# Kernel tuning notes

Hardware: AMD Instinct MI355X
Metric: run time of the kernel (lower is better)

## Reference

```python
import jax, jax.numpy as jnp
import numpy as np

N_NODES = 100000
N_EDGES = 1600000
IN_DIM = 128
HID = 128
EMB = 64


def _glorot(key, shape):
    fan_in, fan_out = shape[0], shape[1]
    lim = np.sqrt(6.0 / (fan_in + fan_out))
    return jax.random.uniform(key, shape, jnp.float32, -lim, lim)


def setup_inputs() -> dict:
    key = jax.random.key(0)
    ks = jax.random.split(key, 16)
    x = jax.random.normal(ks[0], (N_NODES, IN_DIM), jnp.float32)
    src = jax.random.randint(ks[1], (N_EDGES,), 0, N_NODES, jnp.int64)
    dst = jax.random.randint(ks[2], (N_EDGES,), 0, N_NODES, jnp.int64)
    # GCN encoder weights (GraphConv: weight [in,out], bias [out])
    W1 = _glorot(ks[3], (IN_DIM, HID)); b1 = jnp.zeros((HID,), jnp.float32)
    W2 = _glorot(ks[4], (HID, EMB)); b2 = jnp.zeros((EMB,), jnp.float32)
    # MLP predictor: 2*EMB=128 -> 64 -> 32 -> 1
    Wp1 = _glorot(ks[5], (2 * EMB, 64)); bp1 = jnp.zeros((64,), jnp.float32)
    Wp2 = _glorot(ks[6], (64, 32)); bp2 = jnp.zeros((32,), jnp.float32)
    Wp3 = _glorot(ks[7], (32, 1)); bp3 = jnp.zeros((1,), jnp.float32)
    return {"x": x, "src": src, "dst": dst,
            "W1": W1, "b1": b1, "W2": W2, "b2": b2,
            "Wp1": Wp1, "bp1": bp1, "Wp2": Wp2, "bp2": bp2,
            "Wp3": Wp3, "bp3": bp3}


def _gcn_conv(x, src, dst, W, b, n_nodes):
    # DGL GraphConv, norm='both': symmetric degree normalization, sum aggregation.
    ones = jnp.ones((src.shape[0],), x.dtype)
    deg_out = jnp.clip(jax.ops.segment_sum(ones, src, num_segments=n_nodes), 1.0)
    deg_in = jnp.clip(jax.ops.segment_sum(ones, dst, num_segments=n_nodes), 1.0)
    h = (x * jax.lax.rsqrt(deg_out)[:, None]) @ W          # [N, out]
    agg = jax.ops.segment_sum(h[src], dst, num_segments=n_nodes)  # gather + scatter-add
    return agg * jax.lax.rsqrt(deg_in)[:, None] + b


def reference(x, src, dst, W1, b1, W2, b2, Wp1, bp1, Wp2, bp2, Wp3, bp3):
    n = x.shape[0]
    h = jax.nn.relu(_gcn_conv(x, src, dst, W1, b1, n))   # layer 1 (with activation)
    h = _gcn_conv(h, src, dst, W2, b2, n)                # layer 2 (no activation)
    # edge-wise concat of endpoint embeddings: [E, 2*EMB]
    emb = jnp.concatenate([h[src], h[dst]], axis=1)
    z = jax.nn.relu(emb @ Wp1 + bp1)
    z = jax.nn.relu(z @ Wp2 + bp2)
    score = z @ Wp3 + bp3                                # [E, 1]
    return jax.nn.sigmoid(score)
```

## Files before the change

### kernel.cpp

```cpp
#include <hip/hip_runtime.h>
#include <math.h>


#define NBLK 256
#define NBUK 512
#define GRD (NBUK * NBLK)
#define GRT (2 * GRD)

typedef __attribute__((ext_vector_type(8))) short bf16x8;
typedef __attribute__((ext_vector_type(4))) float f32x4;

__device__ __forceinline__ float bl(unsigned u) { return __uint_as_float(u << 16); }
__device__ __forceinline__ float bh(unsigned u) { return __uint_as_float(u & 0xffff0000u); }
__device__ __forceinline__ unsigned short f2bf(float f) {
  unsigned u = __float_as_uint(f);
  return (unsigned short)((u + 0x7fffu + ((u >> 16) & 1u)) >> 16);
}
__device__ __forceinline__ unsigned packbf2(float a, float b) {
  return (unsigned)f2bf(a) | ((unsigned)f2bf(b) << 16);
}


__global__ __launch_bounds__(256) void k_hist(
    const int* __restrict__ src, const int* __restrict__ dst,
    int* __restrict__ grams, int E,
    const float* __restrict__ W1, const float* __restrict__ W2,
    const float* __restrict__ Wp1, const float* __restrict__ Wp2,
    unsigned short* __restrict__ W1t, unsigned short* __restrict__ W2t,
    unsigned short* __restrict__ Wct, unsigned short* __restrict__ Wp2t) {
  __shared__ int hd[NBUK], hs[NBUK];
  int blk = blockIdx.x, t = threadIdx.x;
  {
    int i = blk * 256 + t;
    if (i < 16384) {
      int n = i >> 7, k = i & 127;
      W1t[i] = f2bf(W1[k * 128 + n]);
    } else if (i < 24576) {
      int j = i - 16384; int n = j >> 7, k = j & 127;
      W2t[j] = f2bf(W2[k * 64 + n]);
    } else if (i < 32768) {
      int j = i - 24576; int c = j >> 6, k = j & 63;
      float v = (c < 64) ? Wp1[k * 64 + c] : Wp1[(k + 64) * 64 + (c - 64)];
      Wct[j] = f2bf(v);
    } else if (i < 34816) {
      int j = i - 32768; int n = j >> 6, k = j & 63;
      Wp2t[j] = f2bf(Wp2[k * 32 + n]);
    }
  }
  for (int k = t; k < NBUK; k += 256) { hd[k] = 0; hs[k] = 0; }
  __syncthreads();
  int chunk = (E + NBLK - 1) / NBLK;
  int start = blk * chunk, end = min(E, start + chunk);
  for (int i = start + t; i < end; i += 256) {
    atomicAdd(&hd[dst[i] >> 8], 1);
    atomicAdd(&hs[src[i] >> 8], 1);
  }
  __syncthreads();
  for (int k = t; k < NBUK; k += 256) {
    grams[k * NBLK + blk] = hd[k];
    grams[GRD + k * NBLK + blk] = hs[k];
  }
}

__global__ __launch_bounds__(256) void k_gscan1(const int* __restrict__ g,
                                                int* __restrict__ bsum) {
  __shared__ int lds[256];
  int b = blockIdx.x, t = threadIdx.x;
  int base = b * 1024 + t * 4;
  int s = g[base] + g[base + 1] + g[base + 2] + g[base + 3];
  lds[t] = s; __syncthreads();
  for (int st = 128; st > 0; st >>= 1) {
    if (t < st) lds[t] += lds[t + st];
    __syncthreads();
  }
  if (t == 0) bsum[b] = lds[0];
}

__global__ __launch_bounds__(256) void k_gscan3(int* __restrict__ g,
                                                const int* __restrict__ bsum) {
  __shared__ int lds[256], lds2[256];
  int b = blockIdx.x, t = threadIdx.x;
  int bv = bsum[t];
  lds2[t] = bv; __syncthreads();
  for (int st = 1; st < 256; st <<= 1) {
    int add = (t >= st) ? lds2[t - st] : 0;
    __syncthreads();
    lds2[t] += add;
    __syncthreads();
  }
  int bpref = (b > 0) ? lds2[b - 1] : 0;

  int base = b * 1024 + t * 4;
  int v[4]; int s = 0;
#pragma unroll
  for (int j = 0; j < 4; j++) { v[j] = g[base + j]; s += v[j]; }
  lds[t] = s; __syncthreads();
  int mine = s;
  for (int st = 1; st < 256; st <<= 1) {
    int add = (t >= st) ? lds[t - st] : 0;
    __syncthreads();
    lds[t] += add;
    __syncthreads();
  }
  int excl = lds[t] - mine + bpref;
#pragma unroll
  for (int j = 0; j < 4; j++) { g[base + j] = excl; excl += v[j]; }
}

__global__ __launch_bounds__(256) void k_part(
    const int* __restrict__ src, const int* __restrict__ dst,
    const int* __restrict__ grams, unsigned* __restrict__ pdst,
    unsigned char* __restrict__ sbuf, int E) {
  __shared__ int curd[NBUK], curs[NBUK];
  int blk = blockIdx.x, t = threadIdx.x;
  for (int k = t; k < NBUK; k += 256) {
    curd[k] = grams[k * NBLK + blk];
    curs[k] = grams[GRD + k * NBLK + blk] - E;
  }
  __syncthreads();
  int chunk = (E + NBLK - 1) / NBLK;
  int start = blk * chunk, end = min(E, start + chunk);
  for (int i = start + t; i < end; i += 256) {
    int s = src[i], d = dst[i];
    int pd = atomicAdd(&curd[d >> 8], 1);
    pdst[pd] = ((unsigned)s << 8) | (unsigned)(d & 255);
    int ps = atomicAdd(&curs[s >> 8], 1);
    sbuf[ps] = (unsigned char)(s & 255);
  }
}

__global__ __launch_bounds__(256) void k_dcsr(
    const unsigned* __restrict__ pdst, const unsigned char* __restrict__ sbuf,
    const int* __restrict__ grams,
    int* __restrict__ adj, int* __restrict__ rowst,
    float* __restrict__ rin, float* __restrict__ rout, int N, int E) {
  __shared__ int hist[256], cur[256];
  int b = blockIdx.x, t = threadIdx.x;
  int base = grams[b * 256];
  int end  = grams[b * 256 + 256];
  hist[t] = 0; __syncthreads();
  for (int i = base + t; i < end; i += 256)
    atomicAdd(&hist[pdst[i] & 255], 1);
  __syncthreads();
  int cnt = hist[t];
  for (int st = 1; st < 256; st <<= 1) {
    int add = (t >= st) ? hist[t - st] : 0;
    __syncthreads();
    hist[t] += add;
    __syncthreads();
  }
  int excl = hist[t] - cnt;
  cur[t] = excl;
  int node = b * 256 + t;
  if (node < N) {
    rowst[node] = base + excl;
    rin[node] = rsqrtf((float)max(cnt, 1));
  }
  __syncthreads();
  for (int i = base + t; i < end; i += 256) {
    unsigned u = pdst[i];
    int pos = base + atomicAdd(&cur[u & 255], 1);
    adj[pos] = (int)(u >> 8);
  }
  __syncthreads();
  hist[t] = 0; __syncthreads();
  int sb = grams[GRD + b * 256] - E;
  int se = grams[GRD + b * 256 + 256] - E;
  for (int i = sb + t; i < se; i += 256)
    atomicAdd(&hist[sbuf[i]], 1);
  __syncthreads();
  if (node < N) rout[node] = rsqrtf((float)max(hist[t], 1));
}

template <int K, int BN, bool ABF, bool SC>
__global__ __launch_bounds__(256) void k_gemm(
    const void* __restrict__ Av, const float* __restrict__ scale,
    const unsigned short* __restrict__ Wt, unsigned short* __restrict__ C, int M) {
  constexpr int KP = K + 8;
  __shared__ __attribute__((aligned(16))) unsigned short As[64][KP];
  __shared__ __attribute__((aligned(16))) unsigned short Ws[BN][KP];
  int tid = threadIdx.x;
  int row0 = blockIdx.x * 64;

  for (int i = tid; i < BN * K / 8; i += 256) {
    int n = i / (K / 8), seg = i % (K / 8);
    *(uint4*)&Ws[n][seg * 8] = ((const uint4*)Wt)[i];
  }
  {
    constexpr int CH = K / 4;
    int r = tid >> 2, q = tid & 3;
    int row = row0 + r;
    if (row < M) {
      float sc = SC ? scale[row] : 1.0f;
      if constexpr (!ABF) {
        const float4* ap = (const float4*)((const float*)Av + (size_t)row * K + q * CH);
#pragma unroll
        for (int c = 0; c < CH / 8; c++) {
          float4 v0 = ap[2 * c], v1 = ap[2 * c + 1];
          uint4 o;
          o.x = packbf2(v0.x * sc, v0.y * sc);
          o.y = packbf2(v0.z * sc, v0.w * sc);
          o.z = packbf2(v1.x * sc, v1.y * sc);
          o.w = packbf2(v1.z * sc, v1.w * sc);
          *(uint4*)&As[r][q * CH + c * 8] = o;
        }
      } else {
        const uint4* ap = (const uint4*)((const unsigned short*)Av + (size_t)row * K + q * CH);
#pragma unroll
        for (int c = 0; c < CH / 8; c++) {
          uint4 v = ap[c];
          if constexpr (SC) {
            uint4 o;
            o.x = packbf2(bl(v.x) * sc, bh(v.x) * sc);
            o.y = packbf2(bl(v.y) * sc, bh(v.y) * sc);
            o.z = packbf2(bl(v.z) * sc, bh(v.z) * sc);
            o.w = packbf2(bl(v.w) * sc, bh(v.w) * sc);
            *(uint4*)&As[r][q * CH + c * 8] = o;
          } else {
            *(uint4*)&As[r][q * CH + c * 8] = v;
          }
        }
      }
    } else {
#pragma unroll
      for (int c = 0; c < CH / 8; c++)
        *(uint4*)&As[r][q * CH + c * 8] = make_uint4(0, 0, 0, 0);
    }
  }
  __syncthreads();

  constexpr int KS = K / 32;
  constexpr int NT = BN / 16;
  int wav = tid >> 6, lane = tid & 63;
  int quad = lane >> 4, lrow = lane & 15;
  int mb = wav * 16;

  bf16x8 af[KS];
#pragma unroll
  for (int s = 0; s < KS; s++)
    af[s] = *(const bf16x8*)&As[mb + lrow][s * 32 + quad * 8];

  f32x4 acc[NT];
#pragma unroll
  for (int nt = 0; nt < NT; nt++) acc[nt] = (f32x4){0.f, 0.f, 0.f, 0.f};
#pragma unroll
  for (int nt = 0; nt < NT; nt++) {
#pragma unroll
    for (int s = 0; s < KS; s++) {
      bf16x8 bf = *(const bf16x8*)&Ws[nt * 16 + lrow][s * 32 + quad * 8];
      acc[nt] = __builtin_amdgcn_mfma_f32_16x16x32_bf16(af[s], bf, acc[nt], 0, 0, 0);
    }
  }
#pragma unroll
  for (int nt = 0; nt < NT; nt++) {
#pragma unroll
    for (int reg = 0; reg < 4; reg++) {
      int row = row0 + mb + quad * 4 + reg;
      if (row < M) C[(size_t)row * BN + nt * 16 + lrow] = f2bf(acc[nt][reg]);
    }
  }
}

template <int F>
__global__ __launch_bounds__(256) void k_agg(
    const unsigned short* __restrict__ hin, const int* __restrict__ rowst,
    const int* __restrict__ adj, const float* __restrict__ rin,
    const float* __restrict__ bias, unsigned short* __restrict__ hout,
    int N, int E, int do_relu) {
  constexpr int TPN = F / 8;
  constexpr int NPB = 256 / TPN;
  int node = blockIdx.x * NPB + threadIdx.x / TPN;
  int c = threadIdx.x % TPN;
  if (node >= N) return;
  int start = rowst[node];
  int end = (node + 1 < N) ? rowst[node + 1] : E;
  const uint4* h4 = (const uint4*)hin;

  float a[8], b[8];
#pragma unroll
  for (int j = 0; j < 8; j++) { a[j] = 0.f; b[j] = 0.f; }

  int i = start;
  for (; i + 3 < end; i += 4) {
    uint4 w0 = h4[(size_t)adj[i] * TPN + c];
    uint4 w1 = h4[(size_t)adj[i + 1] * TPN + c];
    uint4 w2 = h4[(size_t)adj[i + 2] * TPN + c];
    uint4 w3 = h4[(size_t)adj[i + 3] * TPN + c];
    a[0] += bl(w0.x); a[1] += bh(w0.x); a[2] += bl(w0.y); a[3] += bh(w0.y);
    a[4] += bl(w0.z); a[5] += bh(w0.z); a[6] += bl(w0.w); a[7] += bh(w0.w);
    b[0] += bl(w1.x); b[1] += bh(w1.x); b[2] += bl(w1.y); b[3] += bh(w1.y);
    b[4] += bl(w1.z); b[5] += bh(w1.z); b[6] += bl(w1.w); b[7] += bh(w1.w);
    a[0] += bl(w2.x); a[1] += bh(w2.x); a[2] += bl(w2.y); a[3] += bh(w2.y);
    a[4] += bl(w2.z); a[5] += bh(w2.z); a[6] += bl(w2.w); a[7] += bh(w2.w);
    b[0] += bl(w3.x); b[1] += bh(w3.x); b[2] += bl(w3.y); b[3] += bh(w3.y);
    b[4] += bl(w3.z); b[5] += bh(w3.z); b[6] += bl(w3.w); b[7] += bh(w3.w);
  }
  for (; i < end; i++) {
    uint4 w0 = h4[(size_t)adj[i] * TPN + c];
    a[0] += bl(w0.x); a[1] += bh(w0.x); a[2] += bl(w0.y); a[3] += bh(w0.y);
    a[4] += bl(w0.z); a[5] += bh(w0.z); a[6] += bl(w0.w); a[7] += bh(w0.w);
  }
  float r = rin[node];
  const float4* bp = (const float4*)(bias + c * 8);
  float4 bb0 = bp[0], bb1 = bp[1];
  float o0 = fmaf(a[0] + b[0], r, bb0.x);
  float o1 = fmaf(a[1] + b[1], r, bb0.y);
  float o2 = fmaf(a[2] + b[2], r, bb0.z);
  float o3 = fmaf(a[3] + b[3], r, bb0.w);
  float o4 = fmaf(a[4] + b[4], r, bb1.x);
  float o5 = fmaf(a[5] + b[5], r, bb1.y);
  float o6 = fmaf(a[6] + b[6], r, bb1.z);
  float o7 = fmaf(a[7] + b[7], r, bb1.w);
  if (do_relu) {
    o0 = fmaxf(o0, 0.f); o1 = fmaxf(o1, 0.f); o2 = fmaxf(o2, 0.f);
    o3 = fmaxf(o3, 0.f); o4 = fmaxf(o4, 0.f); o5 = fmaxf(o5, 0.f);
    o6 = fmaxf(o6, 0.f); o7 = fmaxf(o7, 0.f);
  }
  uint4 o;
  o.x = packbf2(o0, o1); o.y = packbf2(o2, o3);
  o.z = packbf2(o4, o5); o.w = packbf2(o6, o7);
  ((uint4*)hout)[(size_t)node * TPN + c] = o;
}

__global__ __launch_bounds__(256) void k_edge(
    const unsigned short* __restrict__ ab, const int* __restrict__ src,
    const int* __restrict__ dst,
    const unsigned short* __restrict__ Wp2t, const float* __restrict__ bp1,
    const float* __restrict__ bp2, const float* __restrict__ Wp3,
    const float* __restrict__ bp3, float* __restrict__ out, int E) {
  __shared__ __attribute__((aligned(16))) unsigned short z1s[128][72];
  __shared__ __attribute__((aligned(16))) unsigned short w2t[32][72];
  __shared__ float sb1[64], sb2[32], sw3[32];

  int t = threadIdx.x;
  {
    uint4 v = ((const uint4*)Wp2t)[t];
    int n = t >> 3, seg = t & 7;
    *(uint4*)&w2t[n][seg * 8] = v;
    if (t < 64) sb1[t] = bp1[t];
    else if (t < 96) sb2[t - 64] = bp2[t - 64];
    else if (t < 128) sw3[t - 96] = Wp3[t - 96];
  }
  __syncthreads();

  int p0 = blockIdx.x * 128;
  {
    int m = t >> 1, half = t & 1, p = p0 + m;
    int s = 0, d = 0;
    if (p < E) { s = src[p]; d = dst[p]; }
    const uint4* apf = (const uint4*)(ab + (size_t)s * 128 + half * 32);
    const uint4* bpf = (const uint4*)(ab + (size_t)d * 128 + 64 + half * 32);
    int jb = half * 32;
#pragma unroll
    for (int q = 0; q < 4; q++) {
      uint4 av = apf[q], bv = bpf[q];
      int j = jb + 8 * q;
      float z0 = fmaxf(bl(av.x) + bl(bv.x) + sb1[j + 0], 0.f);
      float z1 = fmaxf(bh(av.x) + bh(bv.x) + sb1[j + 1], 0.f);
      float z2 = fmaxf(bl(av.y) + bl(bv.y) + sb1[j + 2], 0.f);
      float z3 = fmaxf(bh(av.y) + bh(bv.y) + sb1[j + 3], 0.f);
      float z4 = fmaxf(bl(av.z) + bl(bv.z) + sb1[j + 4], 0.f);
      float z5 = fmaxf(bh(av.z) + bh(bv.z) + sb1[j + 5], 0.f);
      float z6 = fmaxf(bl(av.w) + bl(bv.w) + sb1[j + 6], 0.f);
      float z7 = fmaxf(bh(av.w) + bh(bv.w) + sb1[j + 7], 0.f);
      uint4 o;
      o.x = packbf2(z0, z1); o.y = packbf2(z2, z3);
      o.z = packbf2(z4, z5); o.w = packbf2(z6, z7);
      *(uint4*)&z1s[m][j] = o;
    }
  }
  __syncthreads();

  int wav = t >> 6, lane = t & 63;
  int quad = lane >> 4, lrow = lane & 15;

  bf16x8 bfr[2][2];
#pragma unroll
  for (int s = 0; s < 2; s++)
#pragma unroll
    for (int nt = 0; nt < 2; nt++)
      bfr[s][nt] = *(const bf16x8*)&w2t[nt * 16 + lrow][s * 32 + quad * 8];

  f32x4 acc[2][2];
#pragma unroll
  for (int mt = 0; mt < 2; mt++)
#pragma unroll
    for (int nt = 0; nt < 2; nt++) acc[mt][nt] = (f32x4){0.f, 0.f, 0.f, 0.f};

#pragma unroll
  for (int mt = 0; mt < 2; mt++) {
    int mb = (wav * 2 + mt) * 16;
#pragma unroll
    for (int s = 0; s < 2; s++) {
      bf16x8 a = *(const bf16x8*)&z1s[mb + lrow][s * 32 + quad * 8];
#pragma unroll
      for (int nt = 0; nt < 2; nt++)
        acc[mt][nt] = __builtin_amdgcn_mfma_f32_16x16x32_bf16(a, bfr[s][nt], acc[mt][nt], 0, 0, 0);
    }
  }

  float bb0 = sb2[lrow], bb1 = sb2[16 + lrow];
  float w30 = sw3[lrow], w31 = sw3[16 + lrow];
  float p2[2][4];
#pragma unroll
  for (int mt = 0; mt < 2; mt++)
#pragma unroll
    for (int reg = 0; reg < 4; reg++)
      p2[mt][reg] = fmaxf(acc[mt][0][reg] + bb0, 0.f) * w30 +
                    fmaxf(acc[mt][1][reg] + bb1, 0.f) * w31;
#pragma unroll
  for (int off = 1; off < 16; off <<= 1) {
#pragma unroll
    for (int mt = 0; mt < 2; mt++)
#pragma unroll
      for (int reg = 0; reg < 4; reg++)
        p2[mt][reg] += __shfl_xor(p2[mt][reg], off, 64);
  }
  if (lrow < 4) {
    float b3 = bp3[0];
#pragma unroll
    for (int mt = 0; mt < 2; mt++) {
      float score = p2[mt][0];
      if (lrow == 1) score = p2[mt][1];
      if (lrow == 2) score = p2[mt][2];
      if (lrow == 3) score = p2[mt][3];
      score += b3;
      int pp = p0 + (wav * 2 + mt) * 16 + quad * 4 + lrow;
      if (pp < E) out[pp] = 1.0f / (1.0f + __expf(-score));
    }
  }
}

extern "C" void kernel_launch(void* const* d_in, const int* in_sizes, int n_in,
                              void* d_out, int out_size, void* d_ws, size_t ws_size,
                              hipStream_t stream) {
  const float* x   = (const float*)d_in[0];
  const int*   src = (const int*)d_in[1];
  const int*   dst = (const int*)d_in[2];
  const float* W1  = (const float*)d_in[3];
  const float* b1  = (const float*)d_in[4];
  const float* W2  = (const float*)d_in[5];
  const float* b2  = (const float*)d_in[6];
  const float* Wp1 = (const float*)d_in[7];
  const float* bp1 = (const float*)d_in[8];
  const float* Wp2 = (const float*)d_in[9];
  const float* bp2 = (const float*)d_in[10];
  const float* Wp3 = (const float*)d_in[11];
  const float* bp3 = (const float*)d_in[12];
  float* out = (float*)d_out;

  int N = in_sizes[0] / 128;
  int E = in_sizes[1];

  char* w = (char*)d_ws;
  unsigned short* bufA = (unsigned short*)w;
  unsigned* pdst = (unsigned*)w;
  unsigned char* sbuf = (unsigned char*)(w + (size_t)E * 4);
  w += (size_t)N * 128 * 2;
  unsigned short* bufB = (unsigned short*)w; w += (size_t)N * 128 * 2;
  int* grams  = (int*)w;    w += (size_t)GRT * sizeof(int);
  int* bsum   = (int*)w;    w += 256 * sizeof(int);
  int* rowst  = (int*)w;    w += (size_t)N * sizeof(int);
  int* adj    = (int*)w;    w += (size_t)E * sizeof(int);
  float* rin  = (float*)w;  w += (size_t)N * sizeof(float);
  float* rout = (float*)w;  w += (size_t)N * sizeof(float);
  unsigned short* W1t  = (unsigned short*)w; w += 16384 * 2;
  unsigned short* W2t  = (unsigned short*)w; w += 8192 * 2;
  unsigned short* Wct  = (unsigned short*)w; w += 8192 * 2;
  unsigned short* Wp2t = (unsigned short*)w; w += 2048 * 2;

  int nbk = (N + 255) / 256;

  k_hist<<<NBLK, 256, 0, stream>>>(src, dst, grams, E, W1, W2, Wp1, Wp2,
                                   W1t, W2t, Wct, Wp2t);
  k_gscan1<<<GRT / 1024, 256, 0, stream>>>(grams, bsum);
  k_gscan3<<<GRT / 1024, 256, 0, stream>>>(grams, bsum);
  k_part<<<NBLK, 256, 0, stream>>>(src, dst, grams, pdst, sbuf, E);
  k_dcsr<<<nbk, 256, 0, stream>>>(pdst, sbuf, grams, adj, rowst, rin, rout, N, E);

  k_gemm<128, 128, false, true><<<(N + 63) / 64, 256, 0, stream>>>(x, rout, W1t, bufA, N);
  k_agg<128><<<(N + 15) / 16, 256, 0, stream>>>(bufA, rowst, adj, rin, b1, bufB, N, E, 1);
  k_gemm<128, 64, true, true><<<(N + 63) / 64, 256, 0, stream>>>(bufB, rout, W2t, bufA, N);
  k_agg<64><<<(N + 31) / 32, 256, 0, stream>>>(bufA, rowst, adj, rin, b2, bufB, N, E, 0);
  k_gemm<64, 128, true, false><<<(N + 63) / 64, 256, 0, stream>>>(bufB, nullptr, Wct, bufA, N);
  k_edge<<<(E + 127) / 128, 256, 0, stream>>>(bufA, src, dst, Wp2t,
                                              bp1, bp2, Wp3, bp3, out, E);
}
```

Before: 378.5 us.

## Process edge MLP in destination-sorted CSR order and scatter scores back

Result: slower. 395.7 us (+4.6%).

```diff
diff --git a/kernel.cpp b/kernel.cpp
--- a/kernel.cpp
+++ b/kernel.cpp
@@ -109,7 +109,7 @@
 
 __global__ __launch_bounds__(256) void k_part(
     const int* __restrict__ src, const int* __restrict__ dst,
-    const int* __restrict__ grams, unsigned* __restrict__ pdst,
+    const int* __restrict__ grams, uint2* __restrict__ pdst,
     unsigned char* __restrict__ sbuf, int E) {
   __shared__ int curd[NBUK], curs[NBUK];
   int blk = blockIdx.x, t = threadIdx.x;
@@ -123,24 +123,25 @@
   for (int i = start + t; i < end; i += 256) {
     int s = src[i], d = dst[i];
     int pd = atomicAdd(&curd[d >> 8], 1);
-    pdst[pd] = ((unsigned)s << 8) | (unsigned)(d & 255);
+    pdst[pd] = make_uint2((unsigned)s, (unsigned)i | ((unsigned)(d & 255) << 21));
     int ps = atomicAdd(&curs[s >> 8], 1);
     sbuf[ps] = (unsigned char)(s & 255);
   }
 }
 
 __global__ __launch_bounds__(256) void k_dcsr(
-    const unsigned* __restrict__ pdst, const unsigned char* __restrict__ sbuf,
+    const uint2* __restrict__ pdst, const unsigned char* __restrict__ sbuf,
     const int* __restrict__ grams,
-    int* __restrict__ adj, int* __restrict__ rowst,
-    float* __restrict__ rin, float* __restrict__ rout, int N, int E) {
+    int* __restrict__ adj, int* __restrict__ dnode, int* __restrict__ eidx,
+    int* __restrict__ rowst, float* __restrict__ rin, float* __restrict__ rout,
+    int N, int E) {
   __shared__ int hist[256], cur[256];
   int b = blockIdx.x, t = threadIdx.x;
   int base = grams[b * 256];
   int end  = grams[b * 256 + 256];
   hist[t] = 0; __syncthreads();
   for (int i = base + t; i < end; i += 256)
-    atomicAdd(&hist[pdst[i] & 255], 1);
+    atomicAdd(&hist[(pdst[i].y >> 21) & 255], 1);
   __syncthreads();
   int cnt = hist[t];
   for (int st = 1; st < 256; st <<= 1) {
@@ -158,9 +159,13 @@
   }
   __syncthreads();
   for (int i = base + t; i < end; i += 256) {
-    unsigned u = pdst[i];
-    int pos = base + atomicAdd(&cur[u & 255], 1);
-    adj[pos] = (int)(u >> 8);
+    uint2 u = pdst[i];
+    int lo = (u.y >> 21) & 255;
+    int eid = (int)(u.y & 0x1FFFFFu);
+    int pos = base + atomicAdd(&cur[lo], 1);
+    adj[pos] = (int)u.x;
+    dnode[pos] = b * 256 + lo;
+    eidx[pos] = eid;
   }
   __syncthreads();
   hist[t] = 0; __syncthreads();
@@ -323,11 +328,11 @@
 }
 
 __global__ __launch_bounds__(256) void k_edge(
-    const unsigned short* __restrict__ ab, const int* __restrict__ src,
-    const int* __restrict__ dst,
+    const unsigned short* __restrict__ ab, const int* __restrict__ adj,
+    const int* __restrict__ dnode,
     const unsigned short* __restrict__ Wp2t, const float* __restrict__ bp1,
     const float* __restrict__ bp2, const float* __restrict__ Wp3,
-    const float* __restrict__ bp3, float* __restrict__ out, int E) {
+    const float* __restrict__ bp3, float* __restrict__ tmp, int E) {
   __shared__ __attribute__((aligned(16))) unsigned short z1s[128][72];
   __shared__ __attribute__((aligned(16))) unsigned short w2t[32][72];
   __shared__ float sb1[64], sb2[32], sw3[32];
@@ -347,7 +352,7 @@
   {
     int m = t >> 1, half = t & 1, p = p0 + m;
     int s = 0, d = 0;
-    if (p < E) { s = src[p]; d = dst[p]; }
+    if (p < E) { s = adj[p]; d = dnode[p]; }
     const uint4* apf = (const uint4*)(ab + (size_t)s * 128 + half * 32);
     const uint4* bpf = (const uint4*)(ab + (size_t)d * 128 + 64 + half * 32);
     int jb = half * 32;
@@ -426,9 +431,16 @@
       if (lrow == 3) score = p2[mt][3];
       score += b3;
       int pp = p0 + (wav * 2 + mt) * 16 + quad * 4 + lrow;
-      if (pp < E) out[pp] = 1.0f / (1.0f + __expf(-score));
-    }
-  }
+      if (pp < E) tmp[pp] = 1.0f / (1.0f + __expf(-score));
+    }
+  }
+}
+
+__global__ __launch_bounds__(256) void k_perm(
+    const float* __restrict__ tmp, const int* __restrict__ eidx,
+    float* __restrict__ out, int E) {
+  int p = blockIdx.x * 256 + threadIdx.x;
+  if (p < E) out[eidx[p]] = tmp[p];
 }
 
 extern "C" void kernel_launch(void* const* d_in, const int* in_sizes, int n_in,
@@ -454,14 +466,18 @@
 
   char* w = (char*)d_ws;
   unsigned short* bufA = (unsigned short*)w;
-  unsigned* pdst = (unsigned*)w;
-  unsigned char* sbuf = (unsigned char*)(w + (size_t)E * 4);
+  uint2* pdst = (uint2*)w;
+  unsigned char* sbuf = (unsigned char*)(w + (size_t)E * 8);
   w += (size_t)N * 128 * 2;
-  unsigned short* bufB = (unsigned short*)w; w += (size_t)N * 128 * 2;
+  unsigned short* bufB = (unsigned short*)w;
+  float* tmp = (float*)bufB;
+  w += (size_t)N * 128 * 2;
   int* grams  = (int*)w;    w += (size_t)GRT * sizeof(int);
   int* bsum   = (int*)w;    w += 256 * sizeof(int);
   int* rowst  = (int*)w;    w += (size_t)N * sizeof(int);
   int* adj    = (int*)w;    w += (size_t)E * sizeof(int);
+  int* dnode  = (int*)w;    w += (size_t)E * sizeof(int);
+  int* eidx   = (int*)w;    w += (size_t)E * sizeof(int);
   float* rin  = (float*)w;  w += (size_t)N * sizeof(float);
   float* rout = (float*)w;  w += (size_t)N * sizeof(float);
   unsigned short* W1t  = (unsigned short*)w; w += 16384 * 2;
@@ -476,13 +492,15 @@
   k_gscan1<<<GRT / 1024, 256, 0, stream>>>(grams, bsum);
   k_gscan3<<<GRT / 1024, 256, 0, stream>>>(grams, bsum);
   k_part<<<NBLK, 256, 0, stream>>>(src, dst, grams, pdst, sbuf, E);
-  k_dcsr<<<nbk, 256, 0, stream>>>(pdst, sbuf, grams, adj, rowst, rin, rout, N, E);
+  k_dcsr<<<nbk, 256, 0, stream>>>(pdst, sbuf, grams, adj, dnode, eidx,
+                                  rowst, rin, rout, N, E);
 
   k_gemm<128, 128, false, true><<<(N + 63) / 64, 256, 0, stream>>>(x, rout, W1t, bufA, N);
   k_agg<128><<<(N + 15) / 16, 256, 0, stream>>>(bufA, rowst, adj, rin, b1, bufB, N, E, 1);
   k_gemm<128, 64, true, true><<<(N + 63) / 64, 256, 0, stream>>>(bufB, rout, W2t, bufA, N);
   k_agg<64><<<(N + 31) / 32, 256, 0, stream>>>(bufA, rowst, adj, rin, b2, bufB, N, E, 0);
   k_gemm<64, 128, true, false><<<(N + 63) / 64, 256, 0, stream>>>(bufB, nullptr, Wct, bufA, N);
-  k_edge<<<(E + 127) / 128, 256, 0, stream>>>(bufA, src, dst, Wp2t,
-                                              bp1, bp2, Wp3, bp3, out, E);
-}
+  k_edge<<<(E + 127) / 128, 256, 0, stream>>>(bufA, adj, dnode, Wp2t,
+                                              bp1, bp2, Wp3, bp3, tmp, E);
+  k_perm<<<(E + 255) / 256, 256, 0, stream>>>(tmp, eidx, out, E);
+}
```

## Merge layer-1 GEMM with CSR build and move out-degree scaling into aggregation

Applied to the files above, without the earlier changes.

Result: no change. 374.9 us (-1.0%).

```diff
diff --git a/kernel.cpp b/kernel.cpp
--- a/kernel.cpp
+++ b/kernel.cpp
@@ -129,13 +129,13 @@
   }
 }
 
-__global__ __launch_bounds__(256) void k_dcsr(
+__device__ __forceinline__ void dcsr_body(
     const unsigned* __restrict__ pdst, const unsigned char* __restrict__ sbuf,
     const int* __restrict__ grams,
     int* __restrict__ adj, int* __restrict__ rowst,
-    float* __restrict__ rin, float* __restrict__ rout, int N, int E) {
+    float* __restrict__ rin, float* __restrict__ rout, int N, int E, int b) {
   __shared__ int hist[256], cur[256];
-  int b = blockIdx.x, t = threadIdx.x;
+  int t = threadIdx.x;
   int base = grams[b * 256];
   int end  = grams[b * 256 + 256];
   hist[t] = 0; __syncthreads();
@@ -173,14 +173,15 @@
 }
 
 template <int K, int BN, bool ABF, bool SC>
-__global__ __launch_bounds__(256) void k_gemm(
+__device__ __forceinline__ void gemm_body(
     const void* __restrict__ Av, const float* __restrict__ scale,
-    const unsigned short* __restrict__ Wt, unsigned short* __restrict__ C, int M) {
+    const unsigned short* __restrict__ Wt, unsigned short* __restrict__ C,
+    int M, int bid) {
   constexpr int KP = K + 8;
   __shared__ __attribute__((aligned(16))) unsigned short As[64][KP];
   __shared__ __attribute__((aligned(16))) unsigned short Ws[BN][KP];
   int tid = threadIdx.x;
-  int row0 = blockIdx.x * 64;
+  int row0 = bid * 64;
 
   for (int i = tid; i < BN * K / 8; i += 256) {
     int n = i / (K / 8), seg = i % (K / 8);
@@ -261,12 +262,32 @@
   }
 }
 
-template <int F>
+template <int K, int BN, bool ABF, bool SC>
+__global__ __launch_bounds__(256) void k_gemm(
+    const void* __restrict__ Av, const float* __restrict__ scale,
+    const unsigned short* __restrict__ Wt, unsigned short* __restrict__ C, int M) {
+  gemm_body<K, BN, ABF, SC>(Av, scale, Wt, C, M, blockIdx.x);
+}
+
+__global__ __launch_bounds__(256) void k_gdc(
+    const float* __restrict__ x, const unsigned short* __restrict__ W1t,
+    unsigned short* __restrict__ h0, int M, int ngb,
+    const unsigned* __restrict__ pdst, const unsigned char* __restrict__ sbuf,
+    const int* __restrict__ grams, int* __restrict__ adj, int* __restrict__ rowst,
+    float* __restrict__ rin, float* __restrict__ rout, int N, int E) {
+  if ((int)blockIdx.x < ngb)
+    gemm_body<128, 128, false, false>(x, nullptr, W1t, h0, M, blockIdx.x);
+  else
+    dcsr_body(pdst, sbuf, grams, adj, rowst, rin, rout, N, E,
+              (int)blockIdx.x - ngb);
+}
+
+template <int F, bool RS>
 __global__ __launch_bounds__(256) void k_agg(
     const unsigned short* __restrict__ hin, const int* __restrict__ rowst,
     const int* __restrict__ adj, const float* __restrict__ rin,
-    const float* __restrict__ bias, unsigned short* __restrict__ hout,
-    int N, int E, int do_relu) {
+    const float* __restrict__ rout, const float* __restrict__ bias,
+    unsigned short* __restrict__ hout, int N, int E, int do_relu) {
   constexpr int TPN = F / 8;
   constexpr int NPB = 256 / TPN;
   int node = blockIdx.x * NPB + threadIdx.x / TPN;
@@ -282,23 +303,40 @@
 
   int i = start;
   for (; i + 3 < end; i += 4) {
-    uint4 w0 = h4[(size_t)adj[i] * TPN + c];
-    uint4 w1 = h4[(size_t)adj[i + 1] * TPN + c];
-    uint4 w2 = h4[(size_t)adj[i + 2] * TPN + c];
-    uint4 w3 = h4[(size_t)adj[i + 3] * TPN + c];
-    a[0] += bl(w0.x); a[1] += bh(w0.x); a[2] += bl(w0.y); a[3] += bh(w0.y);
-    a[4] += bl(w0.z); a[5] += bh(w0.z); a[6] += bl(w0.w); a[7] += bh(w0.w);
-    b[0] += bl(w1.x); b[1] += bh(w1.x); b[2] += bl(w1.y); b[3] += bh(w1.y);
-    b[4] += bl(w1.z); b[5] += bh(w1.z); b[6] += bl(w1.w); b[7] += bh(w1.w);
-    a[0] += bl(w2.x); a[1] += bh(w2.x); a[2] += bl(w2.y); a[3] += bh(w2.y);
-    a[4] += bl(w2.z); a[5] += bh(w2.z); a[6] += bl(w2.w); a[7] += bh(w2.w);
-    b[0] += bl(w3.x); b[1] += bh(w3.x); b[2] += bl(w3.y); b[3] += bh(w3.y);
-    b[4] += bl(w3.z); b[5] += bh(w3.z); b[6] += bl(w3.w); b[7] += bh(w3.w);
+    int u0 = adj[i], u1 = adj[i + 1], u2 = adj[i + 2], u3 = adj[i + 3];
+    float r0 = RS ? rout[u0] : 1.0f;
+    float r1 = RS ? rout[u1] : 1.0f;
+    float r2 = RS ? rout[u2] : 1.0f;
+    float r3 = RS ? rout[u3] : 1.0f;
+    uint4 w0 = h4[(size_t)u0 * TPN + c];
+    uint4 w1 = h4[(size_t)u1 * TPN + c];
+    uint4 w2 = h4[(size_t)u2 * TPN + c];
+    uint4 w3 = h4[(size_t)u3 * TPN + c];
+    a[0] = fmaf(r0, bl(w0.x), a[0]); a[1] = fmaf(r0, bh(w0.x), a[1]);
+    a[2] = fmaf(r0, bl(w0.y), a[2]); a[3] = fmaf(r0, bh(w0.y), a[3]);
+    a[4] = fmaf(r0, bl(w0.z), a[4]); a[5] = fmaf(r0, bh(w0.z), a[5]);
+    a[6] = fmaf(r0, bl(w0.w), a[6]); a[7] = fmaf(r0, bh(w0.w), a[7]);
+    b[0] = fmaf(r1, bl(w1.x), b[0]); b[1] = fmaf(r1, bh(w1.x), b[1]);
+    b[2] = fmaf(r1, bl(w1.y), b[2]); b[3] = fmaf(r1, bh(w1.y), b[3]);
+    b[4] = fmaf(r1, bl(w1.z), b[4]); b[5] = fmaf(r1, bh(w1.z), b[5]);
+    b[6] = fmaf(r1, bl(w1.w), b[6]); b[7] = fmaf(r1, bh(w1.w), b[7]);
+    a[0] = fmaf(r2, bl(w2.x), a[0]); a[1] = fmaf(r2, bh(w2.x), a[1]);
+    a[2] = fmaf(r2, bl(w2.y), a[2]); a[3] = fmaf(r2, bh(w2.y), a[3]);
+    a[4] = fmaf(r2, bl(w2.z), a[4]); a[5] = fmaf(r2, bh(w2.z), a[5]);
+    a[6] = fmaf(r2, bl(w2.w), a[6]); a[7] = fmaf(r2, bh(w2.w), a[7]);
+    b[0] = fmaf(r3, bl(w3.x), b[0]); b[1] = fmaf(r3, bh(w3.x), b[1]);
+    b[2] = fmaf(r3, bl(w3.y), b[2]); b[3] = fmaf(r3, bh(w3.y), b[3]);
+    b[4] = fmaf(r3, bl(w3.z), b[4]); b[5] = fmaf(r3, bh(w3.z), b[5]);
+    b[6] = fmaf(r3, bl(w3.w), b[6]); b[7] = fmaf(r3, bh(w3.w), b[7]);
   }
   for (; i < end; i++) {
-    uint4 w0 = h4[(size_t)adj[i] * TPN + c];
-    a[0] += bl(w0.x); a[1] += bh(w0.x); a[2] += bl(w0.y); a[3] += bh(w0.y);
-    a[4] += bl(w0.z); a[5] += bh(w0.z); a[6] += bl(w0.w); a[7] += bh(w0.w);
+    int u0 = adj[i];
+    float r0 = RS ? rout[u0] : 1.0f;
+    uint4 w0 = h4[(size_t)u0 * TPN + c];
+    a[0] = fmaf(r0, bl(w0.x), a[0]); a[1] = fmaf(r0, bh(w0.x), a[1]);
+    a[2] = fmaf(r0, bl(w0.y), a[2]); a[3] = fmaf(r0, bh(w0.y), a[3]);
+    a[4] = fmaf(r0, bl(w0.z), a[4]); a[5] = fmaf(r0, bh(w0.z), a[5]);
+    a[6] = fmaf(r0, bl(w0.w), a[6]); a[7] = fmaf(r0, bh(w0.w), a[7]);
   }
   float r = rin[node];
   const float4* bp = (const float4*)(bias + c * 8);
@@ -426,7 +464,8 @@
       if (lrow == 3) score = p2[mt][3];
       score += b3;
       int pp = p0 + (wav * 2 + mt) * 16 + quad * 4 + lrow;
-      if (pp < E) out[pp] = 1.0f / (1.0f + __expf(-score));
+      if (pp < E)
+        __builtin_nontemporal_store(1.0f / (1.0f + __expf(-score)), &out[pp]);
     }
   }
 }
@@ -453,11 +492,11 @@
   int E = in_sizes[1];
 
   char* w = (char*)d_ws;
-  unsigned short* bufA = (unsigned short*)w;
-  unsigned* pdst = (unsigned*)w;
-  unsigned char* sbuf = (unsigned char*)(w + (size_t)E * 4);
-  w += (size_t)N * 128 * 2;
+  unsigned short* bufA = (unsigned short*)w; w += (size_t)N * 128 * 2;
   unsigned short* bufB = (unsigned short*)w; w += (size_t)N * 128 * 2;
+  unsigned* pdst = (unsigned*)w;             w += (size_t)E * 4;
+  unsigned char* sbuf = (unsigned char*)w;   w += (size_t)E;
+  w = (char*)(((size_t)w + 255) & ~(size_t)255);
   int* grams  = (int*)w;    w += (size_t)GRT * sizeof(int);
   int* bsum   = (int*)w;    w += 256 * sizeof(int);
   int* rowst  = (int*)w;    w += (size_t)N * sizeof(int);
@@ -470,19 +509,25 @@
   unsigned short* Wp2t = (unsigned short*)w; w += 2048 * 2;
 
   int nbk = (N + 255) / 256;
+  int ngb = (N + 63) / 64;
 
   k_hist<<<NBLK, 256, 0, stream>>>(src, dst, grams, E, W1, W2, Wp1, Wp2,
                                    W1t, W2t, Wct, Wp2t);
   k_gscan1<<<GRT / 1024, 256, 0, stream>>>(grams, bsum);
   k_gscan3<<<GRT / 1024, 256, 0, stream>>>(grams, bsum);
   k_part<<<NBLK, 256, 0, stream>>>(src, dst, grams, pdst, sbuf, E);
-  k_dcsr<<<nbk, 256, 0, stream>>>(pdst, sbuf, grams, adj, rowst, rin, rout, N, E);
-
-  k_gemm<128, 128, false, true><<<(N + 63) / 64, 256, 0, stream>>>(x, rout, W1t, bufA, N);
-  k_agg<128><<<(N + 15) / 16, 256, 0, stream>>>(bufA, rowst, adj, rin, b1, bufB, N, E, 1);
-  k_gemm<128, 64, true, true><<<(N + 63) / 64, 256, 0, stream>>>(bufB, rout, W2t, bufA, N);
-  k_agg<64><<<(N + 31) / 32, 256, 0, stream>>>(bufA, rowst, adj, rin, b2, bufB, N, E, 0);
-  k_gemm<64, 128, true, false><<<(N + 63) / 64, 256, 0, stream>>>(bufB, nullptr, Wct, bufA, N);
+
+  k_gdc<<<ngb + nbk, 256, 0, stream>>>(x, W1t, bufA, N, ngb,
+                                       pdst, sbuf, grams, adj, rowst,
+                                       rin, rout, N, E);
+  k_agg<128, true><<<(N + 15) / 16, 256, 0, stream>>>(
+      bufA, rowst, adj, rin, rout, b1, bufB, N, E, 1);
+  k_gemm<128, 64, true, true><<<(N + 63) / 64, 256, 0, stream>>>(
+      bufB, rout, W2t, bufA, N);
+  k_agg<64, false><<<(N + 31) / 32, 256, 0, stream>>>(
+      bufA, rowst, adj, rin, rout, b2, bufB, N, E, 0);
+  k_gemm<64, 128, true, false><<<(N + 63) / 64, 256, 0, stream>>>(
+      bufB, nullptr, Wct, bufA, N);
   k_edge<<<(E + 127) / 128, 256, 0, stream>>>(bufA, src, dst, Wp2t,
                                               bp1, bp2, Wp3, bp3, out, E);
 }
```
